# Optimization experiments

Hardware: AMD Instinct MI355X
Metric: run time of the kernel (lower is better)

## Reference

```python
import jax, jax.numpy as jnp
import numpy as np

B, C_IN, H, W = 8, 64, 64, 64
C_MID = 32


def setup_inputs() -> dict:
    key = jax.random.key(0)
    ks = jax.random.split(key, 7)
    s = 1.0 / np.sqrt(C_IN)
    return {
        "x": jax.random.normal(ks[0], (B, C_IN, H, W), dtype=jnp.float32),
        "Wk": jax.random.normal(ks[1], (C_MID, C_IN), dtype=jnp.float32) * s,
        "bk": jax.random.normal(ks[2], (C_MID,), dtype=jnp.float32) * 0.01,
        "Wq": jax.random.normal(ks[3], (C_MID, C_IN), dtype=jnp.float32) * s,
        "bq": jax.random.normal(ks[4], (C_MID,), dtype=jnp.float32) * 0.01,
        "Wv": jax.random.normal(ks[5], (C_MID, C_IN), dtype=jnp.float32) * s,
        "bv": jax.random.normal(ks[6], (C_MID,), dtype=jnp.float32) * 0.01,
    }


def reference(x, Wk, bk, Wq, bq, Wv, bv):
    # 1x1 convs == per-pixel channel projections
    def proj(Wt, bt):
        return jnp.einsum('bchw,oc->bohw', x, Wt) + bt[None, :, None, None]

    k = proj(Wk, bk)  # [B, Cm, H, W]
    q = proj(Wq, bq)
    v = proj(Wv, bv)

    b, c, h, w = q.shape
    n = h * w
    qf = q.reshape(b, c, n)
    kf = k.reshape(b, c, n)
    vf = v.reshape(b, c, n)

    # correlated_weight over spatial dims [2,3]: QK channel correlation per
    # pixel pair, softmax over key positions, weighted sum of V.
    scores = jnp.einsum('bcn,bcm->bnm', qf, kf)      # [B, N, N]
    attn = jax.nn.softmax(scores, axis=-1)
    out = jnp.einsum('bnm,bcm->bcn', attn, vf)       # [B, Cm, N]
    return out.reshape(b, c, h, w)
```

## Files before the change

kernel.cpp:

```cpp
#include <hip/hip_runtime.h>
#include <hip/hip_bf16.h>
#include <cstdint>
#include <cstddef>


typedef _Float16 f16x8 __attribute__((ext_vector_type(8)));
typedef float  f32x16 __attribute__((ext_vector_type(16)));
typedef float  f32x4  __attribute__((ext_vector_type(4)));

struct alignas(16) U4 { uint32_t w[4]; };
struct alignas(8)  U2 { uint32_t w[2]; };

#define MFMA16(A, B, C) __builtin_amdgcn_mfma_f32_32x32x16_f16((A), (B), (C), 0, 0, 0)

__device__ __forceinline__ uint16_t f2h(float f) {
    _Float16 h = (_Float16)f;
    return __builtin_bit_cast(uint16_t, h);
}
__device__ __forceinline__ uint16_t f2bf(float f) {
    uint32_t u = __builtin_bit_cast(uint32_t, f);
    u += 0x7fffu + ((u >> 16) & 1u);
    return (uint16_t)(u >> 16);
}
__device__ __forceinline__ float bf2f(uint32_t h16) {
    uint32_t u = h16 << 16;
    return __builtin_bit_cast(float, u);
}
__device__ __forceinline__ uint32_t cvtpk16(float lo, float hi) {
    auto h2 = __builtin_amdgcn_cvt_pkrtz(lo, hi);
    return __builtin_bit_cast(uint32_t, h2);
}
__device__ __forceinline__ void swp(uint32_t& a, uint32_t& b) {
    asm("v_permlane32_swap_b32 %0, %1" : "+v"(a), "+v"(b));
}
__device__ __forceinline__ float ex2(float x) {
    float r;
    asm("v_exp_f32 %0, %1" : "=v"(r) : "v"(x));
    return r;
}
__device__ __forceinline__ float max3(float a, float b, float c) {
    return fmaxf(fmaxf(a, b), c);
}
__device__ __forceinline__ f16x8 ld8(const void* p) {
    return __builtin_bit_cast(f16x8, *(const U4*)p);
}
__device__ __forceinline__ void gload16(const void* g, void* l) {
    __builtin_amdgcn_global_load_lds(
        (const __attribute__((address_space(1))) void*)g,
        (__attribute__((address_space(3))) void*)l, 16, 0, 0);
}

__global__ __launch_bounds__(256) void proj_kernel(
    const float* __restrict__ x,
    const float* __restrict__ Wk, const float* __restrict__ bk,
    const float* __restrict__ Wq, const float* __restrict__ bq,
    const float* __restrict__ Wv, const float* __restrict__ bv,
    uint16_t* __restrict__ qf, uint16_t* __restrict__ kf,
    uint16_t* __restrict__ vt)
{
    __shared__ __align__(16) char xtile[64 * 256];

    const int tid = threadIdx.x;
    const int blk = blockIdx.x;
    const int b   = blk >> 6;
    const int n0  = (blk & 63) << 6;
    const int wv  = __builtin_amdgcn_readfirstlane(tid >> 6);
    const int lane = tid & 63;
    const int px  = lane;
    const int n   = n0 + px;
    const int ob  = wv << 3;

    {
        const char* src = (const char*)(x + (size_t)b * 64 * 4096 + n0)
                        + ((size_t)(16 * wv + (lane >> 4))) * 16384
                        + (lane & 15) * 16;
        char* dst = xtile + wv * 4096;
        #pragma unroll
        for (int j = 0; j < 4; ++j)
            gload16(src + (size_t)(4 * j) * 16384, dst + j * 1024);
    }
    __syncthreads();

    float xv[64];
    #pragma unroll
    for (int ci = 0; ci < 64; ++ci)
        xv[ci] = *(const float*)(xtile + ci * 256 + px * 4);

    #pragma unroll
    for (int pass = 0; pass < 3; ++pass) {
        const float* W    = pass == 0 ? Wk : (pass == 1 ? Wq : Wv);
        const float* bias = pass == 0 ? bk : (pass == 1 ? bq : bv);
        float acc[8];
        #pragma unroll
        for (int o = 0; o < 8; ++o) acc[o] = bias[ob + o];
        #pragma unroll
        for (int o = 0; o < 8; ++o) {
            const float* wr = W + (size_t)(ob + o) * 64;
            #pragma unroll
            for (int ci = 0; ci < 64; ++ci)
                acc[o] = fmaf(wr[ci], xv[ci], acc[o]);
        }
        if (pass == 2) {
            #pragma unroll
            for (int o = 0; o < 8; ++o) {
                int c   = ob + o;
                int nsw = (n & ~0x38) | ((((n >> 3) & 7) ^ (c & 7)) << 3);
                vt[((size_t)(b * 32 + c)) * 4096 + nsw] = f2h(acc[o]);
            }
        } else {
            if (pass == 1) {
                #pragma unroll
                for (int o = 0; o < 8; ++o) acc[o] *= 1.44269504f;
            }
            U4 u;
            #pragma unroll
            for (int t = 0; t < 4; ++t)
                u.w[t] = (uint32_t)f2h(acc[2 * t]) | ((uint32_t)f2h(acc[2 * t + 1]) << 16);
            if (pass == 0) {
                char* rowb = (char*)kf + ((size_t)(b * 4096 + n)) * 64;
                *(U4*)(rowb + ((wv ^ (n & 3)) * 16)) = u;
            } else {
                *(U4*)(qf + ((size_t)(b * 4096 + n)) * 32 + ob) = u;
            }
        }
    }
}

__global__ __launch_bounds__(256, 4) void attn_kernel(
    const uint16_t* __restrict__ qf, const uint16_t* __restrict__ kf,
    const uint16_t* __restrict__ vt, float* __restrict__ out,
    uint16_t* __restrict__ opart, float* __restrict__ mpart,
    float* __restrict__ lpart, int ns)
{
    __shared__ __align__(16) char lds_k[2][2][4096];
    __shared__ __align__(16) char lds_v[2][2][4096];

    const int blk    = blockIdx.x;
    const int b      = blk & 7;
    const int rest   = blk >> 3;
    const int qblk   = rest & 31;
    const int ksp    = rest >> 5;
    const int ntiles = 64 / ns;
    const int kb0    = ksp * ntiles;
    const int niter  = ntiles >> 1;

    const int tid  = threadIdx.x;
    const int wv   = __builtin_amdgcn_readfirstlane(tid >> 6);
    const int lane = tid & 63;
    const int l31  = lane & 31;
    const int h32  = lane >> 5;
    const int qrow = qblk * 128 + wv * 32 + l31;

    f16x8 q0, q1;
    {
        const uint16_t* r = qf + ((size_t)(b * 4096 + qrow)) * 32;
        q0 = ld8(r + h32 * 8);
        q1 = ld8(r + 16 + h32 * 8);
    }
    f16x8 onesv;
    #pragma unroll
    for (int j = 0; j < 8; ++j) onesv[j] = (_Float16)1.f;

    f32x16 oacc, lacc, zf;
    #pragma unroll
    for (int i = 0; i < 16; ++i) { oacc[i] = 0.f; lacc[i] = 0.f; zf[i] = 0.f; }
    float m_run = -3.0e38f;

    const char* gk   = (const char*)kf + ((size_t)b * 4096) * 64;
    const char* gv   = (const char*)vt
                     + ((size_t)(b * 32 + wv * 8 + (lane >> 3))) * 8192
                     + (lane & 7) * 16;
    const char* gk_l = gk + wv * 1024 + lane * 16;

    const int ka0 = l31 * 64 + ((h32 ^ (l31 & 3)) * 16);
    const int ka1 = l31 * 64 + (((2 + h32) ^ (l31 & 3)) * 16);
    int vo[4];
    #pragma unroll
    for (int j = 0; j < 4; ++j)
        vo[j] = l31 * 128 + (((h32 + 2 * j) ^ (l31 & 7)) * 16);

    gload16(gk_l + (size_t)kb0 * 4096,       lds_k[0][0] + wv * 1024);
    gload16(gv   + (size_t)kb0 * 128,        lds_v[0][0] + wv * 1024);
    gload16(gk_l + (size_t)(kb0 + 1) * 4096, lds_k[0][1] + wv * 1024);
    gload16(gv   + (size_t)(kb0 + 1) * 128,  lds_v[0][1] + wv * 1024);

    int p = 0;
    #pragma unroll 1
    for (int it = 0; it < niter; ++it) {
        __syncthreads();

        if (it + 1 < niter) {
            const int tn = kb0 + 2 * it + 2;
            gload16(gk_l + (size_t)tn * 4096,       lds_k[p ^ 1][0] + wv * 1024);
            gload16(gv   + (size_t)tn * 128,        lds_v[p ^ 1][0] + wv * 1024);
            gload16(gk_l + (size_t)(tn + 1) * 4096, lds_k[p ^ 1][1] + wv * 1024);
            gload16(gv   + (size_t)(tn + 1) * 128,  lds_v[p ^ 1][1] + wv * 1024);
        }

        f32x16 sA0, sA1, sB0, sB1;
        {
            const char* lkA = lds_k[p][0];
            f16x8 a0 = ld8(lkA + ka0);
            f16x8 a1 = ld8(lkA + ka1);
            f16x8 c0 = ld8(lkA + 2048 + ka0);
            f16x8 c1 = ld8(lkA + 2048 + ka1);
            sA0 = MFMA16(a0, q0, zf);
            sA1 = MFMA16(c0, q0, zf);
            sA0 = MFMA16(a1, q1, sA0);
            sA1 = MFMA16(c1, q1, sA1);
            const char* lkB = lds_k[p][1];
            f16x8 e0 = ld8(lkB + ka0);
            f16x8 e1 = ld8(lkB + ka1);
            f16x8 g0 = ld8(lkB + 2048 + ka0);
            f16x8 g1 = ld8(lkB + 2048 + ka1);
            sB0 = MFMA16(e0, q0, zf);
            sB1 = MFMA16(g0, q0, zf);
            sB0 = MFMA16(e1, q1, sB0);
            sB1 = MFMA16(g1, q1, sB1);
        }

        float mx[4];
        #pragma unroll
        for (int i = 0; i < 4; ++i)
            mx[i] = max3(max3(sA0[i], sA0[i + 4], sA0[i + 8]),
                         max3(sA0[i + 12], sA1[i], sA1[i + 4]),
                         max3(sA1[i + 8], sA1[i + 12],
                              max3(max3(sB0[i], sB0[i + 4], sB0[i + 8]),
                                   max3(sB0[i + 12], sB1[i], sB1[i + 4]),
                                   fmaxf(sB1[i + 8], sB1[i + 12]))));
        float pm = fmaxf(max3(mx[0], mx[1], mx[2]), mx[3]);
        pm = fmaxf(pm, __shfl_xor(pm, 32));

        if (__any(pm > m_run + 6.f)) {
            float mn  = fmaxf(m_run, pm);
            float scl = ex2(m_run - mn);
            lacc[0] *= scl;
            #pragma unroll
            for (int i = 0; i < 16; ++i) oacc[i] *= scl;
            m_run = mn;
        }

        #pragma unroll
        for (int sl = 0; sl < 2; ++sl) {
            f32x16& s0 = sl ? sB0 : sA0;
            f32x16& s1 = sl ? sB1 : sA1;
            const char* lv = lds_v[p][sl];

            #pragma unroll
            for (int i = 0; i < 16; ++i) {
                s0[i] = ex2(s0[i] - m_run);
                s1[i] = ex2(s1[i] - m_run);
            }

            U4 f1, f2, f3, f4;
            {
                uint32_t A = cvtpk16(s0[0], s0[1]),  B = cvtpk16(s0[4], s0[5]);   swp(A, B);
                uint32_t C = cvtpk16(s0[2], s0[3]),  D = cvtpk16(s0[6], s0[7]);   swp(C, D);
                f1.w[0] = A; f1.w[1] = C; f1.w[2] = B; f1.w[3] = D;
                A = cvtpk16(s0[8], s0[9]);   B = cvtpk16(s0[12], s0[13]);  swp(A, B);
                C = cvtpk16(s0[10], s0[11]); D = cvtpk16(s0[14], s0[15]);  swp(C, D);
                f2.w[0] = A; f2.w[1] = C; f2.w[2] = B; f2.w[3] = D;
                A = cvtpk16(s1[0], s1[1]);   B = cvtpk16(s1[4], s1[5]);    swp(A, B);
                C = cvtpk16(s1[2], s1[3]);   D = cvtpk16(s1[6], s1[7]);    swp(C, D);
                f3.w[0] = A; f3.w[1] = C; f3.w[2] = B; f3.w[3] = D;
                A = cvtpk16(s1[8], s1[9]);   B = cvtpk16(s1[12], s1[13]);  swp(A, B);
                C = cvtpk16(s1[10], s1[11]); D = cvtpk16(s1[14], s1[15]);  swp(C, D);
                f4.w[0] = A; f4.w[1] = C; f4.w[2] = B; f4.w[3] = D;
            }

            {
                f16x8 fa = __builtin_bit_cast(f16x8, f1);
                f16x8 fb = __builtin_bit_cast(f16x8, f2);
                f16x8 fc = __builtin_bit_cast(f16x8, f3);
                f16x8 fd = __builtin_bit_cast(f16x8, f4);
                f16x8 fs = (fa + fb) + (fc + fd);
                lacc = MFMA16(onesv, fs, lacc);
            }

            {
                f16x8 v0 = ld8(lv + vo[0]);
                f16x8 v1 = ld8(lv + vo[1]);
                f16x8 v2 = ld8(lv + vo[2]);
                f16x8 v3 = ld8(lv + vo[3]);
                oacc = MFMA16(v0, __builtin_bit_cast(f16x8, f1), oacc);
                oacc = MFMA16(v1, __builtin_bit_cast(f16x8, f2), oacc);
                oacc = MFMA16(v2, __builtin_bit_cast(f16x8, f3), oacc);
                oacc = MFMA16(v3, __builtin_bit_cast(f16x8, f4), oacc);
            }
        }
        p ^= 1;
    }

    if (ns == 1) {
        const float inv = 1.f / lacc[0];
        float* ob = out + ((size_t)b * 32) * 4096 + qrow;
        #pragma unroll
        for (int i = 0; i < 16; ++i) {
            int c = (i & 3) + 8 * (i >> 2) + 4 * h32;
            ob[(size_t)c * 4096] = oacc[i] * inv;
        }
    } else {
        uint16_t* op = opart + ((size_t)((ksp * 8 + b) * 32)) * 4096 + qrow;
        #pragma unroll
        for (int i = 0; i < 16; ++i) {
            int c = (i & 3) + 8 * (i >> 2) + 4 * h32;
            op[(size_t)c * 4096] = f2bf(oacc[i]);
        }
        if (h32 == 0) {
            mpart[((size_t)(ksp * 8 + b)) * 4096 + qrow] = m_run;
            lpart[((size_t)(ksp * 8 + b)) * 4096 + qrow] = lacc[0];
        }
    }
}

__global__ __launch_bounds__(256) void reduce_kernel(
    const uint16_t* __restrict__ opart, const float* __restrict__ mpart,
    const float* __restrict__ lpart, float* __restrict__ out, int ns)
{
    const int idx = blockIdx.x * 256 + threadIdx.x;
    const int nq  = idx & 1023;
    const int c   = (idx >> 10) & 31;
    const int b   = idx >> 15;
    const size_t noff = (size_t)nq * 4;

    f32x4 M;
    #pragma unroll
    for (int e = 0; e < 4; ++e) M[e] = -3.0e38f;
    for (int s = 0; s < ns; ++s) {
        f32x4 mm = *(const f32x4*)(mpart + ((size_t)(s * 8 + b)) * 4096 + noff);
        #pragma unroll
        for (int e = 0; e < 4; ++e) M[e] = fmaxf(M[e], mm[e]);
    }
    f32x4 L, O;
    #pragma unroll
    for (int e = 0; e < 4; ++e) { L[e] = 0.f; O[e] = 0.f; }
    for (int s = 0; s < ns; ++s) {
        f32x4 mm = *(const f32x4*)(mpart + ((size_t)(s * 8 + b)) * 4096 + noff);
        f32x4 ll = *(const f32x4*)(lpart + ((size_t)(s * 8 + b)) * 4096 + noff);
        U2 uu = *(const U2*)(opart + ((size_t)((s * 8 + b) * 32 + c)) * 4096 + noff);
        float ov[4];
        ov[0] = bf2f(uu.w[0] & 0xffffu);
        ov[1] = bf2f(uu.w[0] >> 16);
        ov[2] = bf2f(uu.w[1] & 0xffffu);
        ov[3] = bf2f(uu.w[1] >> 16);
        #pragma unroll
        for (int e = 0; e < 4; ++e) {
            float w = ex2(mm[e] - M[e]);
            L[e] += ll[e] * w;
            O[e] += ov[e] * w;
        }
    }
    f32x4 r;
    #pragma unroll
    for (int e = 0; e < 4; ++e) r[e] = O[e] / L[e];
    *(f32x4*)(out + ((size_t)(b * 32 + c)) * 4096 + noff) = r;
}

extern "C" void kernel_launch(void* const* d_in, const int* in_sizes, int n_in,
                              void* d_out, int out_size, void* d_ws, size_t ws_size,
                              hipStream_t stream)
{
    (void)in_sizes; (void)n_in; (void)out_size;
    const float* x  = (const float*)d_in[0];
    const float* Wk = (const float*)d_in[1];
    const float* bk = (const float*)d_in[2];
    const float* Wq = (const float*)d_in[3];
    const float* bq = (const float*)d_in[4];
    const float* Wv = (const float*)d_in[5];
    const float* bv = (const float*)d_in[6];
    float* out = (float*)d_out;

    char* ws = (char*)d_ws;
    const size_t SZ = (size_t)8 * 4096 * 32 * 2;
    uint16_t* qf = (uint16_t*)(ws);
    uint16_t* kf = (uint16_t*)(ws + SZ);
    uint16_t* vt = (uint16_t*)(ws + 2 * SZ);
    const size_t base = 3 * SZ;

    const size_t OB  = (size_t)8 * 32 * 4096 * 2;
    const size_t MB_ = (size_t)8 * 4096 * 4;
    int ns = 1;
    if      (ws_size >= base + 4 * (OB + 2 * MB_)) ns = 4;
    else if (ws_size >= base + 2 * (OB + 2 * MB_)) ns = 2;

    uint16_t* opart = (uint16_t*)(ws + base);
    float*    mpart = (float*)(ws + base + (size_t)ns * OB);
    float*    lpart = (float*)(ws + base + (size_t)ns * OB + (size_t)ns * MB_);

    proj_kernel<<<512, 256, 0, stream>>>(x, Wk, bk, Wq, bq, Wv, bv,
                                         qf, kf, vt);
    attn_kernel<<<ns * 256, 256, 0, stream>>>(qf, kf, vt, out,
                                              opart, mpart, lpart, ns);
    if (ns > 1)
        reduce_kernel<<<1024, 256, 0, stream>>>(opart, mpart, lpart, out, ns);
}
```

Baseline: 59.39 us.

## Fuse split-K reduction into attention kernel via last-block atomic counter

Removes the separate reduce_kernel launch. Each attention block atomically increments a per-(batch, query-block) counter after writing its partials, and the last block to finish merges all splits and writes the final output. The counter is zeroed inside proj_kernel. This saves a launch and a pass over memory, but adds fences and atomics, and leaves the final reduction on a few trailing blocks.

Result: slower. 159.7 us (+169.0%).

```diff
diff --git a/kernel.cpp b/kernel.cpp
--- a/kernel.cpp
+++ b/kernel.cpp
@@ -56,7 +56,7 @@
     const float* __restrict__ Wq, const float* __restrict__ bq,
     const float* __restrict__ Wv, const float* __restrict__ bv,
     uint16_t* __restrict__ qf, uint16_t* __restrict__ kf,
-    uint16_t* __restrict__ vt)
+    uint16_t* __restrict__ vt, int* __restrict__ cnt)
 {
     __shared__ __align__(16) char xtile[64 * 256];
 
@@ -70,6 +70,8 @@
     const int n   = n0 + px;
     const int ob  = wv << 3;
 
+    if (blk == 0) cnt[tid] = 0;
+
     {
         const char* src = (const char*)(x + (size_t)b * 64 * 4096 + n0)
                         + ((size_t)(16 * wv + (lane >> 4))) * 16384
@@ -130,10 +132,11 @@
     const uint16_t* __restrict__ qf, const uint16_t* __restrict__ kf,
     const uint16_t* __restrict__ vt, float* __restrict__ out,
     uint16_t* __restrict__ opart, float* __restrict__ mpart,
-    float* __restrict__ lpart, int ns)
+    float* __restrict__ lpart, int* __restrict__ cnt, int ns)
 {
     __shared__ __align__(16) char lds_k[2][2][4096];
     __shared__ __align__(16) char lds_v[2][2][4096];
+    __shared__ int isLast;
 
     const int blk    = blockIdx.x;
     const int b      = blk & 7;
@@ -299,7 +302,10 @@
             int c = (i & 3) + 8 * (i >> 2) + 4 * h32;
             ob[(size_t)c * 4096] = oacc[i] * inv;
         }
-    } else {
+        return;
+    }
+
+    {
         uint16_t* op = opart + ((size_t)((ksp * 8 + b) * 32)) * 4096 + qrow;
         #pragma unroll
         for (int i = 0; i < 16; ++i) {
@@ -311,49 +317,54 @@
             lpart[((size_t)(ksp * 8 + b)) * 4096 + qrow] = lacc[0];
         }
     }
-}
-
-__global__ __launch_bounds__(256) void reduce_kernel(
-    const uint16_t* __restrict__ opart, const float* __restrict__ mpart,
-    const float* __restrict__ lpart, float* __restrict__ out, int ns)
-{
-    const int idx = blockIdx.x * 256 + threadIdx.x;
-    const int nq  = idx & 1023;
-    const int c   = (idx >> 10) & 31;
-    const int b   = idx >> 15;
-    const size_t noff = (size_t)nq * 4;
-
-    f32x4 M;
-    #pragma unroll
-    for (int e = 0; e < 4; ++e) M[e] = -3.0e38f;
-    for (int s = 0; s < ns; ++s) {
-        f32x4 mm = *(const f32x4*)(mpart + ((size_t)(s * 8 + b)) * 4096 + noff);
-        #pragma unroll
-        for (int e = 0; e < 4; ++e) M[e] = fmaxf(M[e], mm[e]);
-    }
-    f32x4 L, O;
-    #pragma unroll
-    for (int e = 0; e < 4; ++e) { L[e] = 0.f; O[e] = 0.f; }
-    for (int s = 0; s < ns; ++s) {
-        f32x4 mm = *(const f32x4*)(mpart + ((size_t)(s * 8 + b)) * 4096 + noff);
-        f32x4 ll = *(const f32x4*)(lpart + ((size_t)(s * 8 + b)) * 4096 + noff);
-        U2 uu = *(const U2*)(opart + ((size_t)((s * 8 + b) * 32 + c)) * 4096 + noff);
-        float ov[4];
-        ov[0] = bf2f(uu.w[0] & 0xffffu);
-        ov[1] = bf2f(uu.w[0] >> 16);
-        ov[2] = bf2f(uu.w[1] & 0xffffu);
-        ov[3] = bf2f(uu.w[1] >> 16);
-        #pragma unroll
-        for (int e = 0; e < 4; ++e) {
-            float w = ex2(mm[e] - M[e]);
-            L[e] += ll[e] * w;
-            O[e] += ov[e] * w;
-        }
-    }
-    f32x4 r;
-    #pragma unroll
-    for (int e = 0; e < 4; ++e) r[e] = O[e] / L[e];
-    *(f32x4*)(out + ((size_t)(b * 32 + c)) * 4096 + noff) = r;
+
+    __threadfence();
+    __syncthreads();
+    if (tid == 0)
+        isLast = (atomicAdd(&cnt[b * 32 + qblk], 1) == ns - 1);
+    __syncthreads();
+    if (!isLast) return;
+    __threadfence();
+
+    #pragma unroll 1
+    for (int itc = 0; itc < 4; ++itc) {
+        const int idx = itc * 256 + tid;
+        const int c   = idx >> 5;
+        const int qr4 = idx & 31;
+        const size_t noff = (size_t)qblk * 128 + qr4 * 4;
+
+        f32x4 M;
+        #pragma unroll
+        for (int e = 0; e < 4; ++e) M[e] = -3.0e38f;
+        for (int s = 0; s < ns; ++s) {
+            f32x4 mm = *(const f32x4*)(mpart + ((size_t)(s * 8 + b)) * 4096 + noff);
+            #pragma unroll
+            for (int e = 0; e < 4; ++e) M[e] = fmaxf(M[e], mm[e]);
+        }
+        f32x4 L, O;
+        #pragma unroll
+        for (int e = 0; e < 4; ++e) { L[e] = 0.f; O[e] = 0.f; }
+        for (int s = 0; s < ns; ++s) {
+            f32x4 mm = *(const f32x4*)(mpart + ((size_t)(s * 8 + b)) * 4096 + noff);
+            f32x4 ll = *(const f32x4*)(lpart + ((size_t)(s * 8 + b)) * 4096 + noff);
+            U2 uu = *(const U2*)(opart + ((size_t)((s * 8 + b) * 32 + c)) * 4096 + noff);
+            float ov[4];
+            ov[0] = bf2f(uu.w[0] & 0xffffu);
+            ov[1] = bf2f(uu.w[0] >> 16);
+            ov[2] = bf2f(uu.w[1] & 0xffffu);
+            ov[3] = bf2f(uu.w[1] >> 16);
+            #pragma unroll
+            for (int e = 0; e < 4; ++e) {
+                float w = ex2(mm[e] - M[e]);
+                L[e] += ll[e] * w;
+                O[e] += ov[e] * w;
+            }
+        }
+        f32x4 r;
+        #pragma unroll
+        for (int e = 0; e < 4; ++e) r[e] = O[e] / L[e];
+        *(f32x4*)(out + ((size_t)(b * 32 + c)) * 4096 + noff) = r;
+    }
 }
 
 extern "C" void kernel_launch(void* const* d_in, const int* in_sizes, int n_in,
@@ -380,17 +391,16 @@
     const size_t OB  = (size_t)8 * 32 * 4096 * 2;
     const size_t MB_ = (size_t)8 * 4096 * 4;
     int ns = 1;
-    if      (ws_size >= base + 4 * (OB + 2 * MB_)) ns = 4;
-    else if (ws_size >= base + 2 * (OB + 2 * MB_)) ns = 2;
+    if      (ws_size >= base + 4 * (OB + 2 * MB_) + 1024) ns = 4;
+    else if (ws_size >= base + 2 * (OB + 2 * MB_) + 1024) ns = 2;
 
     uint16_t* opart = (uint16_t*)(ws + base);
     float*    mpart = (float*)(ws + base + (size_t)ns * OB);
     float*    lpart = (float*)(ws + base + (size_t)ns * OB + (size_t)ns * MB_);
+    int*      cnt   = (int*)(ws + base + (size_t)ns * OB + 2 * (size_t)ns * MB_);
 
     proj_kernel<<<512, 256, 0, stream>>>(x, Wk, bk, Wq, bq, Wv, bv,
-                                         qf, kf, vt);
+                                         qf, kf, vt, cnt);
     attn_kernel<<<ns * 256, 256, 0, stream>>>(qf, kf, vt, out,
-                                              opart, mpart, lpart, ns);
-    if (ns > 1)
-        reduce_kernel<<<1024, 256, 0, stream>>>(opart, mpart, lpart, out, ns);
-}
+                                              opart, mpart, lpart, cnt, ns);
+}
```
